# Kernel optimization log

Hardware: AMD Instinct MI355X
Metric: run time of the kernel (lower is better)

## Reference

```python
import jax, jax.numpy as jnp
import numpy as np
import math

B, S, D, H = 2, 2048, 1024, 16
HD = D // H  # head_dim = 64
ROPE_BASE = 100000
EPS = 1e-09


def _linear_init(key, in_f, out_f):
    std = min(1.0, math.sqrt(out_f / in_f)) / math.sqrt(in_f)
    return jax.random.normal(key, (in_f, out_f)) * std


def setup_inputs() -> dict:
    key = jax.random.key(0)
    ks = jax.random.split(key, 7)
    Q = jax.random.normal(ks[0], (B, S, D), dtype=jnp.float32)
    K = jax.random.normal(ks[1], (B, S, D), dtype=jnp.float32)
    V = jax.random.normal(ks[2], (B, S, D), dtype=jnp.float32)
    mask = jnp.tril(jnp.ones((S, S), dtype=bool))  # causal
    Wq = _linear_init(ks[3], D, D)
    Wk = _linear_init(ks[4], D, D)
    Wv = _linear_init(ks[5], D, D)
    Wo = _linear_init(ks[6], D, D)
    return {"Q": Q, "K": K, "V": V, "mask": mask,
            "Wq": Wq, "Wk": Wk, "Wv": Wv, "Wo": Wo}


def _rope_tables(seq_len, d):
    positions = jnp.arange(0, seq_len)
    freqs = ROPE_BASE ** (jnp.arange(0, d, 2) / d)
    gamma = positions[:, None] * (1.0 / freqs)[None, :]  # [t, d/2]
    return jnp.cos(gamma).astype(jnp.bfloat16), jnp.sin(gamma).astype(jnp.bfloat16)


def _apply_rope(x, cos, sin):
    # x: [..., t, d]; cos/sin: [t, d/2]
    d = x.shape[-1]
    x1, x2 = x[..., : d // 2], x[..., d // 2:]
    y1 = x1 * cos + x2 * sin
    y2 = -x1 * sin + x2 * cos
    return jnp.concatenate([y1, y2], axis=-1)


def _rms_norm(x):
    rms = jnp.sqrt(jnp.mean(jnp.square(x), axis=-1, keepdims=True) + EPS)
    return x / rms


def reference(Q, K, V, mask, Wq, Wk, Wv, Wo):
    cos, sin = _rope_tables(S, HD)
    q = jnp.dot(Q, Wq)
    k = jnp.dot(K, Wk)
    v = jnp.dot(V, Wv)
    # [B, S, D] -> [B, H, S, HD]
    split = lambda t: t.reshape(*t.shape[:-1], H, HD).swapaxes(-3, -2)
    q, k, v = split(q), split(k), split(v)
    q = _rms_norm(_apply_rope(q, cos, sin))
    k = _rms_norm(_apply_rope(k, cos, sin))
    logits = jnp.einsum('bhqd,bhkd->bhqk', q, k) / jnp.sqrt(jnp.float32(HD))
    logits = jnp.where(mask[None, None, :, :], logits, -1000000000.0)
    attn = jax.nn.softmax(logits, axis=-1)
    vals = jnp.einsum('bhqk,bhkd->bhqd', attn, v)
    # [B, H, S, HD] -> [B, S, D]
    vals = vals.swapaxes(-3, -2).reshape(B, S, D)
    return jnp.dot(vals, Wo)
```

## Files before the change

kernel.cpp:

```cpp
#include <hip/hip_runtime.h>
#include <hip/hip_bf16.h>
#include <stdint.h>

typedef __hip_bfloat16 bf16;
typedef __attribute__((ext_vector_type(8))) short short8;
typedef __attribute__((ext_vector_type(4))) short short4v;
typedef __attribute__((ext_vector_type(4))) float float4v;

static constexpr int nB = 2, nS = 2048, nD = 1024, nH = 16, nHD = 64;
static constexpr int nBS = nB * nS;

#define AS_GLOBAL __attribute__((address_space(1)))
#define AS_LDS    __attribute__((address_space(3)))

union Frag16B { short8 v; uint4 u4; uint2 u2[2]; };

__device__ __forceinline__ void gload_lds16(const void* g, void* l) {
  __builtin_amdgcn_global_load_lds((AS_GLOBAL uint32_t*)(g), (AS_LDS uint32_t*)(l), 16, 0, 0);
}

__device__ __forceinline__ float fast_exp2(float x) {
#if __has_builtin(__builtin_amdgcn_exp2f)
  return __builtin_amdgcn_exp2f(x);
#else
  float r; asm volatile("v_exp_f32 %0, %1" : "=v"(r) : "v"(x)); return r;
#endif
}

__device__ __forceinline__ void lds_barrier() {
  asm volatile("s_waitcnt lgkmcnt(0)\ns_barrier" ::: "memory");
}

__device__ __forceinline__ void lgkm_wait() {
  asm volatile("s_waitcnt lgkmcnt(0)" ::: "memory");
}

__global__ __launch_bounds__(256) void prep_kernel(
    const float* __restrict__ Qin, const float* __restrict__ Kin, const float* __restrict__ Vin,
    const float* __restrict__ Wq, const float* __restrict__ Wk,
    const float* __restrict__ Wv, const float* __restrict__ Wo,
    bf16* __restrict__ Qbf, bf16* __restrict__ Kbf, bf16* __restrict__ Vbf,
    bf16* __restrict__ WqT, bf16* __restrict__ WkT, bf16* __restrict__ WvT, bf16* __restrict__ WoT,
    bf16* __restrict__ cos_t, bf16* __restrict__ sin_t) {
  __shared__ float tile[64][65];
  int bx = blockIdx.x, t = threadIdx.x;
  if (bx < 3072) {
    int tz = bx >> 10, blk = bx & 1023;
    const float* src = tz == 0 ? Qin : tz == 1 ? Kin : Vin;
    bf16* dst = tz == 0 ? Qbf : tz == 1 ? Kbf : Vbf;
#pragma unroll
    for (int i = 0; i < 4; ++i) {
      int idx = blk * 1024 + i * 256 + t;
      float4 v = ((const float4*)src)[idx];
      union { bf16 b[4]; uint2 u; } tmp;
      tmp.b[0] = __float2bfloat16(v.x);
      tmp.b[1] = __float2bfloat16(v.y);
      tmp.b[2] = __float2bfloat16(v.z);
      tmp.b[3] = __float2bfloat16(v.w);
      ((uint2*)dst)[idx] = tmp.u;
    }
  } else if (bx < 4096) {
    int idx = bx - 3072;
    int z = idx >> 8;
    const float* W = z == 0 ? Wq : z == 1 ? Wk : z == 2 ? Wv : Wo;
    bf16* T = z == 0 ? WqT : z == 1 ? WkT : z == 2 ? WvT : WoT;
    int tk = (idx & 15) * 64, tn = ((idx >> 4) & 15) * 64;
    int c = t & 63, r0 = t >> 6;
#pragma unroll
    for (int i = 0; i < 16; ++i) {
      int r = i * 4 + r0;
      tile[r][c] = W[(size_t)(tk + r) * nD + tn + c];
    }
    __syncthreads();
#pragma unroll
    for (int i = 0; i < 16; ++i) {
      int r = i * 4 + r0;
      T[(size_t)(tn + r) * nD + tk + c] = __float2bfloat16(tile[c][r]);
    }
  } else {
    int base = (bx - 4096) * 1024 + t * 4;
#pragma unroll
    for (int i = 0; i < 4; ++i) {
      int e = base + i;
      int s = e >> 5, j = e & 31;
      float inv_freq = powf(100000.0f, -(float)(2 * j) / 64.0f);
      float g = (float)s * inv_freq;
      cos_t[e] = __float2bfloat16(cosf(g));
      sin_t[e] = __float2bfloat16(sinf(g));
    }
  }
}

__global__ __launch_bounds__(512, 2) void gemm_qkv_kernel(
    const bf16* __restrict__ A0, const bf16* __restrict__ A1, const bf16* __restrict__ A2,
    const bf16* __restrict__ Bt0, const bf16* __restrict__ Bt1, const bf16* __restrict__ Bt2,
    bf16* __restrict__ q_h, bf16* __restrict__ k_h, bf16* __restrict__ vt_h,
    const bf16* __restrict__ cos_t, const bf16* __restrict__ sin_t) {
  const int z = blockIdx.z;
  const bf16* __restrict__ A  = z == 0 ? A0 : (z == 1 ? A1 : A2);
  const bf16* __restrict__ Bt = z == 0 ? Bt0 : (z == 1 ? Bt1 : Bt2);

  __shared__ bf16 As[2 * 256 * 32];
  __shared__ bf16 Bs[2 * 256 * 32];

  const int t = threadIdx.x;
  const int lane = t & 63;
  const int wid = t >> 6;
  const int quad = lane >> 4;
  const int l16 = lane & 15;
  const int wm = wid >> 2;
  const int wn = wid & 3;
  const int m0 = blockIdx.x * 256;
  const int n0 = blockIdx.y * 256;

  const int sc    = (t & 7) ^ ((t >> 3) & 7);
  const int sml   = 2 * (t >> 3) + (sc >> 2);
  const int skoff = (sc & 3) * 8;
  const int swave = wid * 512;

  const int R0a = wm * 64 + (l16 >> 1);
  const int R0b = wn * 32 + (l16 >> 1);
  const int cpar = (l16 & 1) * 4;
  const int abase = R0a * 64 + (((cpar + quad) ^ (R0a & 7)) * 8);
  const int bbase = R0b * 64 + (((cpar + quad) ^ (R0b & 7)) * 8);

#define STAGE_A(KT, BUF) do { \
    const bf16* ag_ = A + (size_t)(m0 + sml) * nD + (KT) * 32 + skoff; \
    gload_lds16(ag_, As + (BUF) + swave); \
    gload_lds16(ag_ + (size_t)128 * nD, As + (BUF) + 4096 + swave); \
  } while (0)
#define STAGE_B(KT, BUF) do { \
    const bf16* bg_ = Bt + (size_t)(n0 + sml) * nD + (KT) * 32 + skoff; \
    gload_lds16(bg_, Bs + (BUF) + swave); \
    gload_lds16(bg_ + (size_t)128 * nD, Bs + (BUF) + 4096 + swave); \
  } while (0)

  float4v acc[8][4] = {};

  STAGE_A(0, 0);
  STAGE_B(0, 0);
  STAGE_A(1, 8192);
  asm volatile("s_waitcnt vmcnt(2)" ::: "memory");
  __builtin_amdgcn_s_barrier();

#pragma unroll 2
  for (int T = 0; T < 32; ++T) {
    const int cu = (T & 1) * 8192;
    const int nx = cu ^ 8192;

    if (T < 31) STAGE_B(T + 1, nx);
    Frag16B fa[4], fb[4];
#pragma unroll
    for (int mi = 0; mi < 4; ++mi) fa[mi].u4 = *(const uint4*)&As[cu + abase + mi * 512];
#pragma unroll
    for (int ni = 0; ni < 4; ++ni) fb[ni].u4 = *(const uint4*)&Bs[cu + bbase + ni * 512];
    __builtin_amdgcn_s_setprio(1);
#pragma unroll
    for (int mi = 0; mi < 4; ++mi)
#pragma unroll
      for (int ni = 0; ni < 4; ++ni)
        acc[mi][ni] = __builtin_amdgcn_mfma_f32_16x16x32_bf16(fa[mi].v, fb[ni].v, acc[mi][ni], 0, 0, 0);
    __builtin_amdgcn_s_setprio(0);
    __builtin_amdgcn_s_barrier();

    Frag16B fa2[4];
#pragma unroll
    for (int mi = 0; mi < 4; ++mi) fa2[mi].u4 = *(const uint4*)&As[cu + abase + (mi + 4) * 512];
    asm volatile("s_waitcnt lgkmcnt(0)" ::: "memory");
    __builtin_amdgcn_s_setprio(1);
#pragma unroll
    for (int mi = 0; mi < 2; ++mi)
#pragma unroll
      for (int ni = 0; ni < 4; ++ni)
        acc[4 + mi][ni] = __builtin_amdgcn_mfma_f32_16x16x32_bf16(fa2[mi].v, fb[ni].v, acc[4 + mi][ni], 0, 0, 0);
    __builtin_amdgcn_s_setprio(0);
    __builtin_amdgcn_s_barrier();

    if (T < 30) STAGE_A(T + 2, cu);
    __builtin_amdgcn_s_setprio(1);
#pragma unroll
    for (int mi = 2; mi < 4; ++mi)
#pragma unroll
      for (int ni = 0; ni < 4; ++ni)
        acc[4 + mi][ni] = __builtin_amdgcn_mfma_f32_16x16x32_bf16(fa2[mi].v, fb[ni].v, acc[4 + mi][ni], 0, 0, 0);
    __builtin_amdgcn_s_setprio(0);
    if (T < 30) { asm volatile("s_waitcnt vmcnt(2)" ::: "memory"); }
    else        { asm volatile("s_waitcnt vmcnt(0)" ::: "memory"); }
    __builtin_amdgcn_s_barrier();
  }
#undef STAGE_A
#undef STAGE_B

  const int col0 = n0 + wn * 64;
  if (z <= 1) {
    bf16* dst = z ? k_h : q_h;
#pragma unroll
    for (int mi = 0; mi < 8; ++mi)
#pragma unroll
      for (int r = 0; r < 4; ++r) {
        int row = m0 + wm * 128 + mi * 16 + quad * 4 + r;
        int s = row & (nS - 1);
        float x0 = acc[mi][0][r], x1 = acc[mi][1][r], x2 = acc[mi][2][r], x3 = acc[mi][3][r];
        float y[4];
#pragma unroll
        for (int p = 0; p < 2; ++p) {
          int d = p * 16 + l16;
          float c = __bfloat162float(cos_t[s * 32 + d]);
          float sn = __bfloat162float(sin_t[s * 32 + d]);
          float xa = p ? x1 : x0, xb = p ? x3 : x2;
          y[p] = xa * c + xb * sn;
          y[p + 2] = xb * c - xa * sn;
        }
        float ss = y[0] * y[0] + y[1] * y[1] + y[2] * y[2] + y[3] * y[3];
#pragma unroll
        for (int m = 1; m <= 8; m <<= 1) ss += __shfl_xor(ss, m, 64);
        float inv = 1.0f / sqrtf(ss * (1.0f / 64.0f) + 1e-9f);
#pragma unroll
        for (int ni = 0; ni < 4; ++ni)
          dst[(size_t)row * nD + col0 + ni * 16 + l16] = __float2bfloat16(y[ni] * inv);
      }
  } else {
#pragma unroll
    for (int mi = 0; mi < 8; ++mi)
#pragma unroll
      for (int r = 0; r < 4; ++r) {
        int row = m0 + wm * 128 + mi * 16 + quad * 4 + r;
        int b = row >> 11, s = row & (nS - 1);
#pragma unroll
        for (int ni = 0; ni < 4; ++ni) {
          int col = col0 + ni * 16 + l16;
          int h = col >> 6, d = col & 63;
          vt_h[((size_t)((b * nH + h) * 64 + d)) * nS + s] = __float2bfloat16(acc[mi][ni][r]);
        }
      }
  }
}

__global__ __launch_bounds__(256) void gemm_out_kernel(
    const bf16* __restrict__ A, const bf16* __restrict__ Bt, float* __restrict__ C) {
  __shared__ bf16 As[64 * 64];
  __shared__ bf16 Bs[128 * 64];
  const int t = threadIdx.x;
  const int lane = t & 63;
  const int wid = t >> 6;
  const int quad = lane >> 4;
  const int l16 = lane & 15;
  const int wm = wid >> 1;
  const int wn = wid & 1;
  const int m0 = blockIdx.x * 64;
  const int n0 = blockIdx.y * 128;
  const int K = nD;
  const int rloc = lane >> 3, cl = lane & 7;
  const int cg = cl ^ rloc;

  float4v acc[2][4] = {};
  for (int kt = 0; kt < K; kt += 64) {
    __syncthreads();
#pragma unroll
    for (int p = 0; p < 2; ++p) {
      int rowbase = (p * 4 + wid) * 8;
      gload_lds16(A + (size_t)(m0 + rowbase + rloc) * K + kt + cg * 8, As + (size_t)rowbase * 64);
    }
#pragma unroll
    for (int p = 0; p < 4; ++p) {
      int rowbase = (p * 4 + wid) * 8;
      gload_lds16(Bt + (size_t)(n0 + rowbase + rloc) * K + kt + cg * 8, Bs + (size_t)rowbase * 64);
    }
    __syncthreads();

#pragma unroll
    for (int ks = 0; ks < 2; ++ks) {
      Frag16B a[2], b[4];
#pragma unroll
      for (int mi = 0; mi < 2; ++mi) {
        int row = wm * 32 + mi * 16 + l16;
        int ch = (ks * 4 + quad) ^ (row & 7);
        a[mi].u4 = *(const uint4*)&As[row * 64 + ch * 8];
      }
#pragma unroll
      for (int ni = 0; ni < 4; ++ni) {
        int row = wn * 64 + ni * 16 + l16;
        int ch = (ks * 4 + quad) ^ (row & 7);
        b[ni].u4 = *(const uint4*)&Bs[row * 64 + ch * 8];
      }
#pragma unroll
      for (int mi = 0; mi < 2; ++mi)
#pragma unroll
        for (int ni = 0; ni < 4; ++ni)
          acc[mi][ni] = __builtin_amdgcn_mfma_f32_16x16x32_bf16(a[mi].v, b[ni].v, acc[mi][ni], 0, 0, 0);
    }
  }
#pragma unroll
  for (int mi = 0; mi < 2; ++mi)
#pragma unroll
    for (int ni = 0; ni < 4; ++ni)
#pragma unroll
      for (int r = 0; r < 4; ++r) {
        int row = m0 + wm * 32 + mi * 16 + quad * 4 + r;
        int col = n0 + wn * 64 + ni * 16 + l16;
        C[(size_t)row * nD + col] = acc[mi][ni][r];
      }
}

static constexpr float SC = 0.18033688011112042f;

__global__ __launch_bounds__(256, 2) void attn_kernel(const bf16* __restrict__ q_h,
                                                      const bf16* __restrict__ k_h,
                                                      const bf16* __restrict__ vt_h,
                                                      bf16* __restrict__ vals) {
  __shared__ bf16 lds_buf[4 * 4096];

  const int t = threadIdx.x;
  const int lane = t & 63, wid = t >> 6, quad = lane >> 4, l16 = lane & 15;
  const int id = blockIdx.x;
  const int xcd = id & 7;
  const int j = id >> 3;
  const int jj = j & 31;
  const int bh = xcd * 4 + (jj & 3);
  const int u = jj >> 2;
  const int qt = (j < 32) ? (15 - u) : u;
  const int b = bh >> 4, h = bh & 15;

  const bf16* Kbase = k_h + ((size_t)b * nS) * nD + h * 64;
  const bf16* Vbase = vt_h + (size_t)bh * 64 * nS;

  const int row0 = t >> 3;
  const int cl = t & 7;
  const int cg = cl ^ (row0 & 7);
  const int r7 = l16 & 7;

  bf16* const scratch = lds_buf + wid * 1152;

  const int nkt = 2 * qt + 2;
  const int q0w = qt * 128 + wid * 32;

  Frag16B qf[2][2];
#pragma unroll
  for (int qs = 0; qs < 2; ++qs) {
    const bf16* qp = q_h + ((size_t)(b * nS + q0w + qs * 16 + l16)) * nD + h * 64;
    qf[qs][0].u4 = *(const uint4*)(qp + quad * 8);
    qf[qs][1].u4 = *(const uint4*)(qp + 32 + quad * 8);
  }

  uint4 kreg[2], vreg[2];
#pragma unroll
  for (int i = 0; i < 2; ++i) {
    kreg[i] = *(const uint4*)(Kbase + (size_t)(row0 + i * 32) * nD + cg * 8);
    vreg[i] = *(const uint4*)(Vbase + (size_t)(row0 + i * 32) * nS + cg * 8);
  }

  float4v o_acc[2][4] = {};
  float l_acc[2] = {0.f, 0.f};

  for (int kt = 0; kt < nkt; ++kt) {
    bf16* Kb = lds_buf + (kt & 1) * 4096;
    bf16* Vb = lds_buf + 8192 + (kt & 1) * 4096;
#pragma unroll
    for (int i = 0; i < 2; ++i) {
      *(uint4*)&Kb[(row0 + i * 32) * 64 + cl * 8] = kreg[i];
      *(uint4*)&Vb[(row0 + i * 32) * 64 + cl * 8] = vreg[i];
    }
    if (kt + 1 < nkt) {
#pragma unroll
      for (int i = 0; i < 2; ++i) {
        kreg[i] = *(const uint4*)(Kbase + (size_t)((kt + 1) * 64 + row0 + i * 32) * nD + cg * 8);
        vreg[i] = *(const uint4*)(Vbase + (size_t)(row0 + i * 32) * nS + (kt + 1) * 64 + cg * 8);
      }
    }
    lds_barrier();

    if (kt * 64 <= q0w + 31) {
      float4v st[2][4];
#pragma unroll
      for (int kt4 = 0; kt4 < 4; ++kt4) {
        int row = kt4 * 16 + l16;
        Frag16B k0, k1;
        k0.u4 = *(const uint4*)&Kb[row * 64 + ((quad ^ r7) * 8)];
        k1.u4 = *(const uint4*)&Kb[row * 64 + (((quad + 4) ^ r7) * 8)];
#pragma unroll
        for (int qs = 0; qs < 2; ++qs) {
          float4v zz = {};
          zz = __builtin_amdgcn_mfma_f32_16x16x32_bf16(k0.v, qf[qs][0].v, zz, 0, 0, 0);
          st[qs][kt4] = __builtin_amdgcn_mfma_f32_16x16x32_bf16(k1.v, qf[qs][1].v, zz, 0, 0, 0);
        }
      }

      short4v pf[2][4];
      const bool need_mask = (kt * 64 + 63) > q0w;
      if (need_mask) {
#pragma unroll
        for (int qs = 0; qs < 2; ++qs) {
          int qg = q0w + qs * 16 + l16;
#pragma unroll
          for (int kt4 = 0; kt4 < 4; ++kt4) {
            int key0 = kt * 64 + kt4 * 16 + quad * 4;
#pragma unroll
            for (int r = 0; r < 4; ++r) {
              float x = st[qs][kt4][r] * SC;
              if (key0 + r > qg) x = -12000.0f;
              float p = fast_exp2(x);
              l_acc[qs] += p;
              union { bf16 hh; short ss; } cv;
              cv.hh = __float2bfloat16(p);
              pf[qs][kt4][r] = cv.ss;
            }
          }
        }
      } else {
#pragma unroll
        for (int qs = 0; qs < 2; ++qs)
#pragma unroll
          for (int kt4 = 0; kt4 < 4; ++kt4)
#pragma unroll
            for (int r = 0; r < 4; ++r) {
              float p = fast_exp2(st[qs][kt4][r] * SC);
              l_acc[qs] += p;
              union { bf16 hh; short ss; } cv;
              cv.hh = __float2bfloat16(p);
              pf[qs][kt4][r] = cv.ss;
            }
      }

#pragma unroll
      for (int dt = 0; dt < 4; ++dt) {
        int row = dt * 16 + l16;
#pragma unroll
        for (int kt4 = 0; kt4 < 4; ++kt4) {
          int chunk = kt4 * 2 + (quad >> 1);
          union { uint2 u; short4v s; } vv;
          vv.u = *(const uint2*)&Vb[row * 64 + ((chunk ^ r7) * 8) + (quad & 1) * 4];
          o_acc[0][dt] = __builtin_amdgcn_mfma_f32_16x16x16bf16_1k(vv.s, pf[0][kt4], o_acc[0][dt], 0, 0, 0);
          o_acc[1][dt] = __builtin_amdgcn_mfma_f32_16x16x16bf16_1k(vv.s, pf[1][kt4], o_acc[1][dt], 0, 0, 0);
        }
      }
    }
  }

  lds_barrier();
#pragma unroll
  for (int qs = 0; qs < 2; ++qs) {
    float la = l_acc[qs];
    la += __shfl_xor(la, 16, 64);
    la += __shfl_xor(la, 32, 64);
    float inv_l = 1.0f / la;
#pragma unroll
    for (int dt = 0; dt < 4; ++dt) {
      union { bf16 b2[2]; uint u; } p01, p23;
      p01.b2[0] = __float2bfloat16(o_acc[qs][dt][0] * inv_l);
      p01.b2[1] = __float2bfloat16(o_acc[qs][dt][1] * inv_l);
      p23.b2[0] = __float2bfloat16(o_acc[qs][dt][2] * inv_l);
      p23.b2[1] = __float2bfloat16(o_acc[qs][dt][3] * inv_l);
      *(uint*)&scratch[l16 * 72 + dt * 16 + quad * 4] = p01.u;
      *(uint*)&scratch[l16 * 72 + dt * 16 + quad * 4 + 2] = p23.u;
    }
    lgkm_wait();
    uint4 r0 = *(const uint4*)&scratch[l16 * 72 + quad * 16];
    uint4 r1 = *(const uint4*)&scratch[l16 * 72 + quad * 16 + 8];
    int qrow = q0w + qs * 16 + l16;
    bf16* vp = vals + ((size_t)(b * nS + qrow)) * nD + h * 64 + quad * 16;
    *(uint4*)(vp) = r0;
    *(uint4*)(vp + 8) = r1;
    lgkm_wait();
  }
}

extern "C" void kernel_launch(void* const* d_in, const int* in_sizes, int n_in,
                              void* d_out, int out_size, void* d_ws, size_t ws_size,
                              hipStream_t stream) {
  const float* Qin = (const float*)d_in[0];
  const float* Kin = (const float*)d_in[1];
  const float* Vin = (const float*)d_in[2];
  const float* Wq = (const float*)d_in[4];
  const float* Wk = (const float*)d_in[5];
  const float* Wv = (const float*)d_in[6];
  const float* Wo = (const float*)d_in[7];
  float* out = (float*)d_out;

  char* ws = (char*)d_ws;
  const size_t MB = 1u << 20;
  bf16* Qbf = (bf16*)(ws + 0 * MB);
  bf16* Kbf = (bf16*)(ws + 8 * MB);
  bf16* Vbf = (bf16*)(ws + 16 * MB);
  bf16* WqT = (bf16*)(ws + 24 * MB);
  bf16* WkT = (bf16*)(ws + 26 * MB);
  bf16* WvT = (bf16*)(ws + 28 * MB);
  bf16* WoT = (bf16*)(ws + 30 * MB);
  bf16* cos_t = (bf16*)(ws + 32 * MB);
  bf16* sin_t = (bf16*)(ws + 33 * MB);
  bf16* q_h = (bf16*)(ws + 34 * MB);
  bf16* k_h = (bf16*)(ws + 42 * MB);
  bf16* vt_h = (bf16*)(ws + 50 * MB);
  bf16* vals = (bf16*)(ws + 58 * MB);

  prep_kernel<<<4160, 256, 0, stream>>>(Qin, Kin, Vin, Wq, Wk, Wv, Wo,
                                        Qbf, Kbf, Vbf, WqT, WkT, WvT, WoT, cos_t, sin_t);

  gemm_qkv_kernel<<<dim3(16, 4, 3), 512, 0, stream>>>(Qbf, Kbf, Vbf, WqT, WkT, WvT,
                                                      q_h, k_h, vt_h, cos_t, sin_t);

  attn_kernel<<<512, 256, 0, stream>>>(q_h, k_h, vt_h, vals);

  gemm_out_kernel<<<dim3(64, 8), 256, 0, stream>>>(vals, WoT, out);
}
```

Before: 239.8 us.

## Use 8 waves per attention block with direct global-to-LDS K/V staging

Attention blocks grow from 4 to 8 waves, and each wave now handles 16 query rows instead of 32. This halves per-wave register state and raises the number of waves available to hide latency. K/V tiles are staged with global_load_lds into double-buffered LDS instead of going through registers. MFMA sections are wrapped in s_setprio to favour matrix work. The cost is a full vmcnt wait plus a barrier every iteration, and each K/V tile is now reused across 16 rows per wave rather than 32.

```diff
diff --git a/kernel.cpp b/kernel.cpp
--- a/kernel.cpp
+++ b/kernel.cpp
@@ -304,7 +304,7 @@
 
 static constexpr float SC = 0.18033688011112042f;
 
-__global__ __launch_bounds__(256, 2) void attn_kernel(const bf16* __restrict__ q_h,
+__global__ __launch_bounds__(512, 4) void attn_kernel(const bf16* __restrict__ q_h,
                                                       const bf16* __restrict__ k_h,
                                                       const bf16* __restrict__ vt_h,
                                                       bf16* __restrict__ vals) {
@@ -324,103 +324,89 @@
   const bf16* Kbase = k_h + ((size_t)b * nS) * nD + h * 64;
   const bf16* Vbase = vt_h + (size_t)bh * 64 * nS;
 
-  const int row0 = t >> 3;
-  const int cl = t & 7;
-  const int cg = cl ^ (row0 & 7);
+  const int rl = lane >> 3;
+  const int cg8 = ((lane & 7) ^ rl) * 8;
+  const int srow = wid * 8 + rl;
   const int r7 = l16 & 7;
 
   bf16* const scratch = lds_buf + wid * 1152;
 
   const int nkt = 2 * qt + 2;
-  const int q0w = qt * 128 + wid * 32;
-
-  Frag16B qf[2][2];
-#pragma unroll
-  for (int qs = 0; qs < 2; ++qs) {
-    const bf16* qp = q_h + ((size_t)(b * nS + q0w + qs * 16 + l16)) * nD + h * 64;
-    qf[qs][0].u4 = *(const uint4*)(qp + quad * 8);
-    qf[qs][1].u4 = *(const uint4*)(qp + 32 + quad * 8);
-  }
-
-  uint4 kreg[2], vreg[2];
-#pragma unroll
-  for (int i = 0; i < 2; ++i) {
-    kreg[i] = *(const uint4*)(Kbase + (size_t)(row0 + i * 32) * nD + cg * 8);
-    vreg[i] = *(const uint4*)(Vbase + (size_t)(row0 + i * 32) * nS + cg * 8);
-  }
-
-  float4v o_acc[2][4] = {};
-  float l_acc[2] = {0.f, 0.f};
+  const int q0w = qt * 128 + wid * 16;
+
+  Frag16B qf[2];
+  {
+    const bf16* qp = q_h + ((size_t)(b * nS + q0w + l16)) * nD + h * 64;
+    qf[0].u4 = *(const uint4*)(qp + quad * 8);
+    qf[1].u4 = *(const uint4*)(qp + 32 + quad * 8);
+  }
+
+#define STAGE_KV(KT) do { \
+    const int bo_ = ((KT) & 1) * 4096; \
+    gload_lds16(Kbase + (size_t)((KT) * 64 + srow) * nD + cg8, lds_buf + bo_ + wid * 512); \
+    gload_lds16(Vbase + (size_t)srow * nS + (KT) * 64 + cg8, lds_buf + 8192 + bo_ + wid * 512); \
+  } while (0)
+
+  STAGE_KV(0);
+  asm volatile("s_waitcnt vmcnt(0)" ::: "memory");
+  __builtin_amdgcn_s_barrier();
+
+  float4v o_acc[4] = {};
+  float l_acc = 0.f;
 
   for (int kt = 0; kt < nkt; ++kt) {
-    bf16* Kb = lds_buf + (kt & 1) * 4096;
-    bf16* Vb = lds_buf + 8192 + (kt & 1) * 4096;
-#pragma unroll
-    for (int i = 0; i < 2; ++i) {
-      *(uint4*)&Kb[(row0 + i * 32) * 64 + cl * 8] = kreg[i];
-      *(uint4*)&Vb[(row0 + i * 32) * 64 + cl * 8] = vreg[i];
-    }
-    if (kt + 1 < nkt) {
-#pragma unroll
-      for (int i = 0; i < 2; ++i) {
-        kreg[i] = *(const uint4*)(Kbase + (size_t)((kt + 1) * 64 + row0 + i * 32) * nD + cg * 8);
-        vreg[i] = *(const uint4*)(Vbase + (size_t)(row0 + i * 32) * nS + (kt + 1) * 64 + cg * 8);
-      }
-    }
-    lds_barrier();
-
-    if (kt * 64 <= q0w + 31) {
-      float4v st[2][4];
+    if (kt + 1 < nkt) STAGE_KV(kt + 1);
+
+    const bf16* Kb = lds_buf + (kt & 1) * 4096;
+    const bf16* Vb = lds_buf + 8192 + (kt & 1) * 4096;
+
+    if (kt * 64 <= q0w + 15) {
+      float4v st[4];
+      __builtin_amdgcn_s_setprio(1);
 #pragma unroll
       for (int kt4 = 0; kt4 < 4; ++kt4) {
         int row = kt4 * 16 + l16;
         Frag16B k0, k1;
         k0.u4 = *(const uint4*)&Kb[row * 64 + ((quad ^ r7) * 8)];
         k1.u4 = *(const uint4*)&Kb[row * 64 + (((quad + 4) ^ r7) * 8)];
-#pragma unroll
-        for (int qs = 0; qs < 2; ++qs) {
-          float4v zz = {};
-          zz = __builtin_amdgcn_mfma_f32_16x16x32_bf16(k0.v, qf[qs][0].v, zz, 0, 0, 0);
-          st[qs][kt4] = __builtin_amdgcn_mfma_f32_16x16x32_bf16(k1.v, qf[qs][1].v, zz, 0, 0, 0);
-        }
-      }
-
-      short4v pf[2][4];
+        float4v zz = {};
+        zz = __builtin_amdgcn_mfma_f32_16x16x32_bf16(k0.v, qf[0].v, zz, 0, 0, 0);
+        st[kt4] = __builtin_amdgcn_mfma_f32_16x16x32_bf16(k1.v, qf[1].v, zz, 0, 0, 0);
+      }
+      __builtin_amdgcn_s_setprio(0);
+
+      short4v pf[4];
       const bool need_mask = (kt * 64 + 63) > q0w;
       if (need_mask) {
-#pragma unroll
-        for (int qs = 0; qs < 2; ++qs) {
-          int qg = q0w + qs * 16 + l16;
-#pragma unroll
-          for (int kt4 = 0; kt4 < 4; ++kt4) {
-            int key0 = kt * 64 + kt4 * 16 + quad * 4;
-#pragma unroll
-            for (int r = 0; r < 4; ++r) {
-              float x = st[qs][kt4][r] * SC;
-              if (key0 + r > qg) x = -12000.0f;
-              float p = fast_exp2(x);
-              l_acc[qs] += p;
-              union { bf16 hh; short ss; } cv;
-              cv.hh = __float2bfloat16(p);
-              pf[qs][kt4][r] = cv.ss;
-            }
+        int qg = q0w + l16;
+#pragma unroll
+        for (int kt4 = 0; kt4 < 4; ++kt4) {
+          int key0 = kt * 64 + kt4 * 16 + quad * 4;
+#pragma unroll
+          for (int r = 0; r < 4; ++r) {
+            float x = st[kt4][r] * SC;
+            if (key0 + r > qg) x = -12000.0f;
+            float p = fast_exp2(x);
+            l_acc += p;
+            union { bf16 hh; short ss; } cv;
+            cv.hh = __float2bfloat16(p);
+            pf[kt4][r] = cv.ss;
           }
         }
       } else {
 #pragma unroll
-        for (int qs = 0; qs < 2; ++qs)
-#pragma unroll
-          for (int kt4 = 0; kt4 < 4; ++kt4)
-#pragma unroll
-            for (int r = 0; r < 4; ++r) {
-              float p = fast_exp2(st[qs][kt4][r] * SC);
-              l_acc[qs] += p;
-              union { bf16 hh; short ss; } cv;
-              cv.hh = __float2bfloat16(p);
-              pf[qs][kt4][r] = cv.ss;
-            }
-      }
-
+        for (int kt4 = 0; kt4 < 4; ++kt4)
+#pragma unroll
+          for (int r = 0; r < 4; ++r) {
+            float p = fast_exp2(st[kt4][r] * SC);
+            l_acc += p;
+            union { bf16 hh; short ss; } cv;
+            cv.hh = __float2bfloat16(p);
+            pf[kt4][r] = cv.ss;
+          }
+      }
+
+      __builtin_amdgcn_s_setprio(1);
 #pragma unroll
       for (int dt = 0; dt < 4; ++dt) {
         int row = dt * 16 + l16;
@@ -429,39 +415,38 @@
           int chunk = kt4 * 2 + (quad >> 1);
           union { uint2 u; short4v s; } vv;
           vv.u = *(const uint2*)&Vb[row * 64 + ((chunk ^ r7) * 8) + (quad & 1) * 4];
-          o_acc[0][dt] = __builtin_amdgcn_mfma_f32_16x16x16bf16_1k(vv.s, pf[0][kt4], o_acc[0][dt], 0, 0, 0);
-          o_acc[1][dt] = __builtin_amdgcn_mfma_f32_16x16x16bf16_1k(vv.s, pf[1][kt4], o_acc[1][dt], 0, 0, 0);
+          o_acc[dt] = __builtin_amdgcn_mfma_f32_16x16x16bf16_1k(vv.s, pf[kt4], o_acc[dt], 0, 0, 0);
         }
       }
-    }
-  }
-
-  lds_barrier();
-#pragma unroll
-  for (int qs = 0; qs < 2; ++qs) {
-    float la = l_acc[qs];
-    la += __shfl_xor(la, 16, 64);
-    la += __shfl_xor(la, 32, 64);
-    float inv_l = 1.0f / la;
-#pragma unroll
-    for (int dt = 0; dt < 4; ++dt) {
-      union { bf16 b2[2]; uint u; } p01, p23;
-      p01.b2[0] = __float2bfloat16(o_acc[qs][dt][0] * inv_l);
-      p01.b2[1] = __float2bfloat16(o_acc[qs][dt][1] * inv_l);
-      p23.b2[0] = __float2bfloat16(o_acc[qs][dt][2] * inv_l);
-      p23.b2[1] = __float2bfloat16(o_acc[qs][dt][3] * inv_l);
-      *(uint*)&scratch[l16 * 72 + dt * 16 + quad * 4] = p01.u;
-      *(uint*)&scratch[l16 * 72 + dt * 16 + quad * 4 + 2] = p23.u;
-    }
-    lgkm_wait();
-    uint4 r0 = *(const uint4*)&scratch[l16 * 72 + quad * 16];
-    uint4 r1 = *(const uint4*)&scratch[l16 * 72 + quad * 16 + 8];
-    int qrow = q0w + qs * 16 + l16;
-    bf16* vp = vals + ((size_t)(b * nS + qrow)) * nD + h * 64 + quad * 16;
-    *(uint4*)(vp) = r0;
-    *(uint4*)(vp + 8) = r1;
-    lgkm_wait();
-  }
+      __builtin_amdgcn_s_setprio(0);
+    }
+
+    asm volatile("s_waitcnt vmcnt(0) lgkmcnt(0)" ::: "memory");
+    __builtin_amdgcn_s_barrier();
+  }
+#undef STAGE_KV
+
+  float la = l_acc;
+  la += __shfl_xor(la, 16, 64);
+  la += __shfl_xor(la, 32, 64);
+  float inv_l = 1.0f / la;
+#pragma unroll
+  for (int dt = 0; dt < 4; ++dt) {
+    union { bf16 b2[2]; uint u; } p01, p23;
+    p01.b2[0] = __float2bfloat16(o_acc[dt][0] * inv_l);
+    p01.b2[1] = __float2bfloat16(o_acc[dt][1] * inv_l);
+    p23.b2[0] = __float2bfloat16(o_acc[dt][2] * inv_l);
+    p23.b2[1] = __float2bfloat16(o_acc[dt][3] * inv_l);
+    *(uint*)&scratch[l16 * 72 + dt * 16 + quad * 4] = p01.u;
+    *(uint*)&scratch[l16 * 72 + dt * 16 + quad * 4 + 2] = p23.u;
+  }
+  lgkm_wait();
+  uint4 r0 = *(const uint4*)&scratch[l16 * 72 + quad * 16];
+  uint4 r1 = *(const uint4*)&scratch[l16 * 72 + quad * 16 + 8];
+  int qrow = q0w + l16;
+  bf16* vp = vals + ((size_t)(b * nS + qrow)) * nD + h * 64 + quad * 16;
+  *(uint4*)(vp) = r0;
+  *(uint4*)(vp + 8) = r1;
 }
 
 extern "C" void kernel_launch(void* const* d_in, const int* in_sizes, int n_in,
@@ -498,7 +483,7 @@
   gemm_qkv_kernel<<<dim3(16, 4, 3), 512, 0, stream>>>(Qbf, Kbf, Vbf, WqT, WkT, WvT,
                                                       q_h, k_h, vt_h, cos_t, sin_t);
 
-  attn_kernel<<<512, 256, 0, stream>>>(q_h, k_h, vt_h, vals);
+  attn_kernel<<<512, 512, 0, stream>>>(q_h, k_h, vt_h, vals);
 
   gemm_out_kernel<<<dim3(64, 8), 256, 0, stream>>>(vals, WoT, out);
 }
```

Result: faster. 223.2 us (-6.9%).
